# Kernel tuning notes

Hardware: AMD Instinct MI355X
Metric: run time of the kernel (lower is better)

## Reference

```python
import jax, jax.numpy as jnp
from jax import lax
import numpy as np

PAD = 1          # padding (pair, symmetric)
STRIDE = (1, 1)  # (strideY, strideX)
KH, KW = 3, 3
C_IN, C_OUT = 256, 512


def setup_inputs() -> dict:
    key = jax.random.key(0)
    k1, k2 = jax.random.split(key)
    x = jax.random.normal(k1, (1, C_IN, 256, 256), dtype=jnp.float32)
    # reset_parameters: uniform(-stdv, stdv), stdv = 1/sqrt(numel(weight))
    stdv = 1.0 / np.sqrt(C_OUT * C_IN * KH * KW)
    weight = jax.random.uniform(k2, (C_OUT, C_IN, KH, KW), dtype=jnp.float32,
                                minval=-stdv, maxval=stdv)
    return {"x": x, "weight": weight}


def reference(x, weight):
    # pad H and W with constant value 1 (as in module's pad())
    xp = jnp.pad(x, ((0, 0), (0, 0), (PAD, PAD), (PAD, PAD)), constant_values=1.0)
    # binarize input: (x >= 0) -> +1 else -1 (detached in torch; non-diff anyway)
    xb = jnp.where(xp >= 0, 1.0, -1.0).astype(x.dtype)
    # input_K: channel-mean of |x| then avg_pool2d(kernel, stride), VALID
    abs_mean = jnp.mean(jnp.abs(xp), axis=1)  # [B, Hp, Wp]
    k_sum = lax.reduce_window(abs_mean, 0.0, lax.add,
                              (1, KH, KW), (1,) + STRIDE, 'VALID')
    input_K = k_sum / (KH * KW)  # [B, Ho, Wo]
    # binary conv (real-valued emulation of XNOR+popcount)
    conv = lax.conv_general_dilated(xb, weight, window_strides=STRIDE,
                                    padding='VALID',
                                    dimension_numbers=('NCHW', 'OIHW', 'NCHW'))
    # weight_alpha: per-output-channel mean of weight (note: mean, not abs-mean,
    # in the training-path forward())
    alpha = jnp.mean(weight, axis=(1, 2, 3))  # [C_out]
    return conv * input_K[:, None, :, :] * alpha[None, :, None, None]
```

## Files before the change

### kernel.cpp

```cpp
#include <hip/hip_runtime.h>

typedef unsigned short UST;
typedef unsigned int u32;
typedef __attribute__((ext_vector_type(4))) int i32x4;

#define HPAD 258
#define CIN 256
#define COUT 512
#define KTOT 2304

#define SCALES_OFF (COUT * KTOT)
#define XBT_OFF    (SCALES_OFF + 2048)
#define XBT_BYTES  (HPAD * HPAD * CIN)
#define ABSM_OFF   (XBT_OFF + XBT_BYTES)
#define ABSM_BYTES (HPAD * HPAD * 4)
#define INK_OFF    (ABSM_OFF + ABSM_BYTES)

__device__ __forceinline__ void gload_lds16(const void* g, void* l) {
  __builtin_amdgcn_global_load_lds(
      (const __attribute__((address_space(1))) u32*)g,
      (__attribute__((address_space(3))) u32*)l, 16, 0, 0);
}

__global__ __launch_bounds__(256) void k_prep_w(const float* __restrict__ w,
                                                signed char* __restrict__ wq,
                                                float* __restrict__ scales) {
  int co = blockIdx.x;
  int ci = threadIdx.x;
  const float* wr = w + co * KTOT + ci * 9;
  float v[9];
  float s = 0.f, mx = 0.f;
#pragma unroll
  for (int j = 0; j < 9; ++j) {
    v[j] = wr[j]; s += v[j]; mx = fmaxf(mx, fabsf(v[j]));
  }
  __shared__ float redS[256];
  __shared__ float redM[256];
  redS[ci] = s; redM[ci] = mx;
  __syncthreads();
#pragma unroll
  for (int off = 128; off > 0; off >>= 1) {
    if (ci < off) {
      redS[ci] += redS[ci + off];
      redM[ci] = fmaxf(redM[ci], redM[ci + off]);
    }
    __syncthreads();
  }
  float alpha = redS[0] * (1.0f / 2304.0f);
  float maxw = redM[0];
  float inv = 127.0f / maxw;
  signed char* wo = wq + co * KTOT + ci;
#pragma unroll
  for (int j = 0; j < 9; ++j)
    wo[j * 256] = (signed char)__float2int_rn(v[j] * inv);
  if (ci == 0) scales[co] = alpha * maxw * (1.0f / 127.0f);
}

__global__ __launch_bounds__(256) void k_binz(const float* __restrict__ x,
                                              signed char* __restrict__ xbt,
                                              float* __restrict__ absm) {
  int hp = blockIdx.x;
  int wt = blockIdx.y;
  int wpl = threadIdx.x & 63;
  int chunk = threadIdx.x >> 6;
  int wp = wt * 64 + wpl;
  bool valid = wp < HPAD;
  int hx = hp - 1, wx = wp - 1;
  bool inb = valid && ((unsigned)hx < 256u) && ((unsigned)wx < 256u);
  float asum = 0.f;
  u32 pk[16];
#pragma unroll
  for (int c4 = 0; c4 < 16; ++c4) {
    u32 word = 0;
#pragma unroll
    for (int b = 0; b < 4; ++b) {
      int ci = chunk * 64 + c4 * 4 + b;
      float v = 1.0f;
      if (inb) v = x[(unsigned)ci * 65536u + (unsigned)(hx * 256 + wx)];
      asum += fabsf(v);
      u32 byte = (v >= 0.f) ? 0x01u : 0xFFu;
      word |= byte << (8 * b);
    }
    pk[c4] = word;
  }
  if (valid) {
    uint4* dst = (uint4*)(xbt + (unsigned)(hp * HPAD + wp) * 256u + chunk * 64);
#pragma unroll
    for (int g = 0; g < 4; ++g)
      dst[g] = make_uint4(pk[g * 4], pk[g * 4 + 1], pk[g * 4 + 2], pk[g * 4 + 3]);
  }
  __shared__ float red[4][64];
  red[chunk][wpl] = asum;
  __syncthreads();
  if (chunk == 0 && valid) {
    float tot = red[0][wpl] + red[1][wpl] + red[2][wpl] + red[3][wpl];
    absm[hp * HPAD + wp] = tot * (1.0f / 256.0f);
  }
}

__global__ __launch_bounds__(256) void k_inputk(const float* __restrict__ absm,
                                                float* __restrict__ inK) {
  int h = blockIdx.x, w = threadIdx.x;
  float s = 0.f;
#pragma unroll
  for (int dh = 0; dh < 3; ++dh)
#pragma unroll
    for (int dw = 0; dw < 3; ++dw) s += absm[(h + dh) * HPAD + (w + dw)];
  inK[h * 256 + w] = s * (1.0f / 9.0f);
}

#define MMI(a, b, c) __builtin_amdgcn_mfma_i32_16x16x64_i8(a, b, c, 0, 0, 0)

#define A_LDS(BUF) (lds + (BUF) * 32768)
#define B_LDS(BUF) (lds + 65536 + (BUF) * 32768)
#define RD_A(BUF, KS, M) (*(const i32x4*)(A_LDS(BUF) + swzA[KS][M]))
#define RD_B(BUF, KS, N) (*(const i32x4*)(B_LDS(BUF) + swzB[KS][N]))

#define STAGE_A(SRC, BUF) do { \
    char* d_ = A_LDS(BUF) + wv * 1024; \
    gload_lds16((SRC) + aoff[0], d_); \
    gload_lds16((SRC) + aoff[1], d_ + 8192); \
    gload_lds16((SRC) + aoff[2], d_ + 16384); \
    gload_lds16((SRC) + aoff[3], d_ + 24576); } while (0)

#define STAGE_B(SRC, BUF) do { \
    char* d_ = B_LDS(BUF) + wv * 1024; \
    gload_lds16((SRC) + boff[0], d_); \
    gload_lds16((SRC) + boff[1], d_ + 8192); \
    gload_lds16((SRC) + boff[2], d_ + 16384); \
    gload_lds16((SRC) + boff[3], d_ + 24576); } while (0)

#define SB __builtin_amdgcn_sched_barrier(0)

#define RD12(BUF, KS, BV, ALO, AHI) \
  BV[0] = RD_B(BUF, KS, 0); BV[1] = RD_B(BUF, KS, 1); \
  BV[2] = RD_B(BUF, KS, 2); BV[3] = RD_B(BUF, KS, 3); \
  ALO[0] = RD_A(BUF, KS, 0); ALO[1] = RD_A(BUF, KS, 1); \
  ALO[2] = RD_A(BUF, KS, 2); ALO[3] = RD_A(BUF, KS, 3); \
  AHI[0] = RD_A(BUF, KS, 4); AHI[1] = RD_A(BUF, KS, 5); \
  AHI[2] = RD_A(BUF, KS, 6); AHI[3] = RD_A(BUF, KS, 7);

#define MFMA32(ALO, AHI, BV) \
  __builtin_amdgcn_s_setprio(1); \
  _Pragma("unroll") for (int m = 0; m < 4; ++m) \
  _Pragma("unroll") for (int n = 0; n < 4; ++n) \
    acc[m][n] = MMI(ALO[m], BV[n], acc[m][n]); \
  _Pragma("unroll") for (int m = 0; m < 4; ++m) \
  _Pragma("unroll") for (int n = 0; n < 4; ++n) \
    acc[m + 4][n] = MMI(AHI[m], BV[n], acc[m + 4][n]); \
  __builtin_amdgcn_s_setprio(0);

#define BODY(CUR, ASRC, BSRC) do { \
  i32x4 b0[4], alo0[4], ahi0[4], b1[4], alo1[4], ahi1[4]; \
  RD12(CUR, 0, b0, alo0, ahi0); \
  STAGE_A((ASRC), (CUR) ^ 1); STAGE_B((BSRC), (CUR) ^ 1); \
  SB; MFMA32(alo0, ahi0, b0); SB; \
  RD12(CUR, 1, b1, alo1, ahi1); \
  SB; MFMA32(alo1, ahi1, b1); SB; \
  asm volatile("s_waitcnt vmcnt(0)" ::: "memory"); \
  __builtin_amdgcn_s_barrier(); \
} while (0)

#define BODY_LAST(CUR) do { \
  i32x4 b0[4], alo0[4], ahi0[4], b1[4], alo1[4], ahi1[4]; \
  RD12(CUR, 0, b0, alo0, ahi0); \
  SB; MFMA32(alo0, ahi0, b0); SB; \
  RD12(CUR, 1, b1, alo1, ahi1); \
  SB; MFMA32(alo1, ahi1, b1); SB; \
} while (0)

__global__ __launch_bounds__(512, 2) void k_conv8(const signed char* __restrict__ wq,
                                                  const signed char* __restrict__ xbt,
                                                  const float* __restrict__ scales,
                                                  const float* __restrict__ inK,
                                                  float* __restrict__ out) {
  __shared__ __align__(16) char lds[131072];
  int tid = threadIdx.x;
  int lane = tid & 63;
  int wv = tid >> 6;
  int wm = wv >> 2, wn = wv & 3;
  int bid = blockIdx.x;
  int bs = (bid & 7) * 64 + (bid >> 3);
  int mt = bs & 1;
  int h = bs >> 1;
  int co0 = mt << 8;

  int aoff[4], boff[4];
#pragma unroll
  for (int i = 0; i < 4; ++i) {
    u32 ql = (u32)(i * 512 + tid) * 16u;
    u32 row = ql >> 7;
    u32 s = (ql >> 4) & 7u;
    u32 slot = s ^ (row & 7u);
    aoff[i] = (int)((co0 + row) * 2304u + slot * 16u);
    boff[i] = (int)(row * 256u + slot * 16u);
  }
  int swzA[2][8], swzB[2][4];
#pragma unroll
  for (int ks = 0; ks < 2; ++ks) {
#pragma unroll
    for (int m = 0; m < 8; ++m) {
      u32 row = (u32)(wm * 128 + m * 16 + (lane & 15));
      u32 slot = (u32)(ks * 4 + (lane >> 4));
      swzA[ks][m] = (int)(row * 128u + (slot ^ (row & 7u)) * 16u);
    }
#pragma unroll
    for (int n = 0; n < 4; ++n) {
      u32 row = (u32)(wn * 64 + n * 16 + (lane & 15));
      u32 slot = (u32)(ks * 4 + (lane >> 4));
      swzB[ks][n] = (int)(row * 128u + (slot ^ (row & 7u)) * 16u);
    }
  }

  const char* wb_b = (const char*)wq;
  const char* xbt_b = (const char*)xbt;

  i32x4 acc[8][4];
#pragma unroll
  for (int m = 0; m < 8; ++m)
#pragma unroll
    for (int n = 0; n < 4; ++n) acc[m][n] = (i32x4){0, 0, 0, 0};

  STAGE_A(wb_b, 0);
  STAGE_B(xbt_b + (h * HPAD) * 256, 0);
  asm volatile("s_waitcnt vmcnt(0)" ::: "memory");
  __builtin_amdgcn_s_barrier();

#pragma unroll
  for (int t = 0; t < 17; ++t) {
    int tn = t + 1;
    int g = tn >> 1;
    int gh = g / 3, gw = g % 3;
    const char* asrc = wb_b + tn * 128;
    const char* bsrc = xbt_b + ((h + gh) * HPAD + gw) * 256 + (tn & 1) * 128;
    if (t & 1) { BODY(1, asrc, bsrc); }
    else       { BODY(0, asrc, bsrc); }
  }
  BODY_LAST(1);

  int col = lane & 15, rg = lane >> 4;
  int pixbase = h * 256;
#pragma unroll
  for (int n = 0; n < 4; ++n) {
    int w = wn * 64 + n * 16 + col;
    float kv = inK[pixbase + w];
#pragma unroll
    for (int m = 0; m < 8; ++m) {
      int cobase = co0 + wm * 128 + m * 16 + rg * 4;
      float4 scv = *(const float4*)(scales + cobase);
      float* o = out + (u32)cobase * 65536u + (u32)(pixbase + w);
      o[0]          = (float)acc[m][n][0] * scv.x * kv;
      o[65536u]     = (float)acc[m][n][1] * scv.y * kv;
      o[2u * 65536u] = (float)acc[m][n][2] * scv.z * kv;
      o[3u * 65536u] = (float)acc[m][n][3] * scv.w * kv;
    }
  }
}

extern "C" void kernel_launch(void* const* d_in, const int* in_sizes, int n_in,
                              void* d_out, int out_size, void* d_ws, size_t ws_size,
                              hipStream_t stream) {
  const float* x = (const float*)d_in[0];
  const float* w = (const float*)d_in[1];
  float* out = (float*)d_out;
  char* ws = (char*)d_ws;
  signed char* wq = (signed char*)ws;
  float* scales = (float*)(ws + SCALES_OFF);
  signed char* xbt = (signed char*)(ws + XBT_OFF);
  float* absm = (float*)(ws + ABSM_OFF);
  float* inK = (float*)(ws + INK_OFF);

  k_prep_w<<<COUT, 256, 0, stream>>>(w, wq, scales);
  k_binz<<<dim3(HPAD, 5), 256, 0, stream>>>(x, xbt, absm);
  k_inputk<<<256, 256, 0, stream>>>(absm, inK);
  k_conv8<<<512, 512, 0, stream>>>(wq, xbt, scales, inK, out);
}
```

Before: 110.3 us.

## Deepen conv LDS pipeline with triple-buffered B and interleaved fragment reads

Restructures the int8 MFMA main loop in the conv kernel. The B (activation) tile is now triple-buffered in a larger 160KB LDS, and next-step fragment reads are interleaved between MFMA halves. The barrier waits only for older loads (vmcnt(4)) instead of draining all global loads. Because of the larger LDS footprint, launch bounds drop to one 512-thread block per CU, which trades occupancy for deeper prefetch and less stall per step.

After: 108.6 us. Within noise of the previous version (-1.6%).

```diff
diff --git a/kernel.cpp b/kernel.cpp
--- a/kernel.cpp
+++ b/kernel.cpp
@@ -111,70 +111,106 @@
 
 #define MMI(a, b, c) __builtin_amdgcn_mfma_i32_16x16x64_i8(a, b, c, 0, 0, 0)
 
-#define A_LDS(BUF) (lds + (BUF) * 32768)
-#define B_LDS(BUF) (lds + 65536 + (BUF) * 32768)
-#define RD_A(BUF, KS, M) (*(const i32x4*)(A_LDS(BUF) + swzA[KS][M]))
-#define RD_B(BUF, KS, N) (*(const i32x4*)(B_LDS(BUF) + swzB[KS][N]))
-
-#define STAGE_A(SRC, BUF) do { \
-    char* d_ = A_LDS(BUF) + wv * 1024; \
+#define A_LDS(S) (lds + (S) * 32768)
+#define B_LDS(S) (lds + 65536 + (S) * 32768)
+#define RD_A(S, KS, M) (*(const i32x4*)(A_LDS(S) + swzA[KS][M]))
+#define RD_B(S, KS, N) (*(const i32x4*)(B_LDS(S) + swzB[KS][N]))
+
+#define STAGE_A(SRC, S) do { \
+    char* d_ = A_LDS(S) + wv * 1024; \
     gload_lds16((SRC) + aoff[0], d_); \
     gload_lds16((SRC) + aoff[1], d_ + 8192); \
     gload_lds16((SRC) + aoff[2], d_ + 16384); \
     gload_lds16((SRC) + aoff[3], d_ + 24576); } while (0)
 
-#define STAGE_B(SRC, BUF) do { \
-    char* d_ = B_LDS(BUF) + wv * 1024; \
+#define STAGE_B(SRC, S) do { \
+    char* d_ = B_LDS(S) + wv * 1024; \
     gload_lds16((SRC) + boff[0], d_); \
     gload_lds16((SRC) + boff[1], d_ + 8192); \
     gload_lds16((SRC) + boff[2], d_ + 16384); \
     gload_lds16((SRC) + boff[3], d_ + 24576); } while (0)
 
 #define SB __builtin_amdgcn_sched_barrier(0)
-
-#define RD12(BUF, KS, BV, ALO, AHI) \
-  BV[0] = RD_B(BUF, KS, 0); BV[1] = RD_B(BUF, KS, 1); \
-  BV[2] = RD_B(BUF, KS, 2); BV[3] = RD_B(BUF, KS, 3); \
-  ALO[0] = RD_A(BUF, KS, 0); ALO[1] = RD_A(BUF, KS, 1); \
-  ALO[2] = RD_A(BUF, KS, 2); ALO[3] = RD_A(BUF, KS, 3); \
-  AHI[0] = RD_A(BUF, KS, 4); AHI[1] = RD_A(BUF, KS, 5); \
-  AHI[2] = RD_A(BUF, KS, 6); AHI[3] = RD_A(BUF, KS, 7);
-
-#define MFMA32(ALO, AHI, BV) \
+#define VMW(N) asm volatile("s_waitcnt vmcnt(" #N ")" ::: "memory")
+#define LGK0 asm volatile("s_waitcnt lgkmcnt(0)" ::: "memory")
+
+#define RDB4(S, KS, D) \
+  D[0] = RD_B(S, KS, 0); D[1] = RD_B(S, KS, 1); \
+  D[2] = RD_B(S, KS, 2); D[3] = RD_B(S, KS, 3);
+#define RDALO(S, KS, D) \
+  D[0] = RD_A(S, KS, 0); D[1] = RD_A(S, KS, 1); \
+  D[2] = RD_A(S, KS, 2); D[3] = RD_A(S, KS, 3);
+#define RDAHI(S, KS, D) \
+  D[0] = RD_A(S, KS, 4); D[1] = RD_A(S, KS, 5); \
+  D[2] = RD_A(S, KS, 6); D[3] = RD_A(S, KS, 7);
+
+#define MF_LO(AA, BB) \
   __builtin_amdgcn_s_setprio(1); \
   _Pragma("unroll") for (int m = 0; m < 4; ++m) \
   _Pragma("unroll") for (int n = 0; n < 4; ++n) \
-    acc[m][n] = MMI(ALO[m], BV[n], acc[m][n]); \
+    acc[m][n] = MMI(AA[m], BB[n], acc[m][n]); \
+  __builtin_amdgcn_s_setprio(0);
+#define MF_HI(AA, BB) \
+  __builtin_amdgcn_s_setprio(1); \
   _Pragma("unroll") for (int m = 0; m < 4; ++m) \
   _Pragma("unroll") for (int n = 0; n < 4; ++n) \
-    acc[m + 4][n] = MMI(AHI[m], BV[n], acc[m + 4][n]); \
+    acc[m + 4][n] = MMI(AA[m], BB[n], acc[m + 4][n]); \
   __builtin_amdgcn_s_setprio(0);
 
-#define BODY(CUR, ASRC, BSRC) do { \
-  i32x4 b0[4], alo0[4], ahi0[4], b1[4], alo1[4], ahi1[4]; \
-  RD12(CUR, 0, b0, alo0, ahi0); \
-  STAGE_A((ASRC), (CUR) ^ 1); STAGE_B((BSRC), (CUR) ^ 1); \
-  SB; MFMA32(alo0, ahi0, b0); SB; \
-  RD12(CUR, 1, b1, alo1, ahi1); \
-  SB; MFMA32(alo1, ahi1, b1); SB; \
-  asm volatile("s_waitcnt vmcnt(0)" ::: "memory"); \
+#define BGPX(TT) (xbt_b + ((h + ((TT) >> 1) / 3) * HPAD + (((TT) >> 1) % 3)) * 256 \
+                  + ((TT) & 1) * 128)
+
+#define BODY(CA, CB, SA, SBT, TA, TB, ASRC, BSRC) do { \
+  i32x4 Ahi_[4], B1_[4], A1lo_[4], A1hi_[4]; \
+  RDAHI(CA, 0, Ahi_); \
+  STAGE_A((ASRC), SA); STAGE_B((BSRC), SBT); \
+  SB; MF_LO(Alo_, B0_); SB; \
+  RDB4(CB, 1, B1_); RDALO(CA, 1, A1lo_); \
+  SB; MF_HI(Ahi_, B0_); SB; \
+  RDAHI(CA, 1, A1hi_); \
+  SB; MF_LO(A1lo_, B1_); SB; \
+  LGK0; VMW(4); \
   __builtin_amdgcn_s_barrier(); \
+  RDB4(TB, 0, B0_); RDALO(TA, 0, Alo_); \
+  SB; MF_HI(A1hi_, B1_); SB; \
 } while (0)
 
-#define BODY_LAST(CUR) do { \
-  i32x4 b0[4], alo0[4], ahi0[4], b1[4], alo1[4], ahi1[4]; \
-  RD12(CUR, 0, b0, alo0, ahi0); \
-  SB; MFMA32(alo0, ahi0, b0); SB; \
-  RD12(CUR, 1, b1, alo1, ahi1); \
-  SB; MFMA32(alo1, ahi1, b1); SB; \
+#define BU(U) BODY((U) & 1, (U) % 3, ((U) + 1) & 1, ((U) + 2) % 3, \
+                   ((U) + 1) & 1, ((U) + 1) % 3, \
+                   wb_b + ((U) + 1) * 128, BGPX((U) + 2))
+
+#define BODY16() do { \
+  i32x4 Ahi_[4], B1_[4], A1lo_[4], A1hi_[4]; \
+  RDAHI(0, 0, Ahi_); \
+  STAGE_A(wb_b + 17 * 128, 1); \
+  SB; MF_LO(Alo_, B0_); SB; \
+  RDB4(1, 1, B1_); RDALO(0, 1, A1lo_); \
+  SB; MF_HI(Ahi_, B0_); SB; \
+  RDAHI(0, 1, A1hi_); \
+  SB; MF_LO(A1lo_, B1_); SB; \
+  LGK0; VMW(0); \
+  __builtin_amdgcn_s_barrier(); \
+  RDB4(2, 0, B0_); RDALO(1, 0, Alo_); \
+  SB; MF_HI(A1hi_, B1_); SB; \
 } while (0)
 
-__global__ __launch_bounds__(512, 2) void k_conv8(const signed char* __restrict__ wq,
+#define BODY17() do { \
+  i32x4 Ahi_[4], B1_[4], A1lo_[4], A1hi_[4]; \
+  RDAHI(1, 0, Ahi_); \
+  SB; MF_LO(Alo_, B0_); SB; \
+  RDB4(2, 1, B1_); RDALO(1, 1, A1lo_); \
+  SB; MF_HI(Ahi_, B0_); SB; \
+  RDAHI(1, 1, A1hi_); \
+  SB; MF_LO(A1lo_, B1_); SB; \
+  SB; MF_HI(A1hi_, B1_); SB; \
+} while (0)
+
+__global__ __launch_bounds__(512, 1) void k_conv8(const signed char* __restrict__ wq,
                                                   const signed char* __restrict__ xbt,
                                                   const float* __restrict__ scales,
                                                   const float* __restrict__ inK,
                                                   float* __restrict__ out) {
-  __shared__ __align__(16) char lds[131072];
+  __shared__ __align__(16) char lds[163840];
   int tid = threadIdx.x;
   int lane = tid & 63;
   int wv = tid >> 6;
@@ -221,22 +257,19 @@
 #pragma unroll
     for (int n = 0; n < 4; ++n) acc[m][n] = (i32x4){0, 0, 0, 0};
 
+  i32x4 B0_[4], Alo_[4];
+
   STAGE_A(wb_b, 0);
-  STAGE_B(xbt_b + (h * HPAD) * 256, 0);
-  asm volatile("s_waitcnt vmcnt(0)" ::: "memory");
+  STAGE_B(BGPX(0), 0);
+  STAGE_B(BGPX(1), 1);
+  VMW(4);
   __builtin_amdgcn_s_barrier();
-
-#pragma unroll
-  for (int t = 0; t < 17; ++t) {
-    int tn = t + 1;
-    int g = tn >> 1;
-    int gh = g / 3, gw = g % 3;
-    const char* asrc = wb_b + tn * 128;
-    const char* bsrc = xbt_b + ((h + gh) * HPAD + gw) * 256 + (tn & 1) * 128;
-    if (t & 1) { BODY(1, asrc, bsrc); }
-    else       { BODY(0, asrc, bsrc); }
-  }
-  BODY_LAST(1);
+  RDB4(0, 0, B0_); RDALO(0, 0, Alo_);
+
+  BU(0); BU(1); BU(2); BU(3); BU(4); BU(5); BU(6); BU(7);
+  BU(8); BU(9); BU(10); BU(11); BU(12); BU(13); BU(14); BU(15);
+  BODY16();
+  BODY17();
 
   int col = lane & 15, rg = lane >> 4;
   int pixbase = h * 256;
@@ -249,8 +282,8 @@
       int cobase = co0 + wm * 128 + m * 16 + rg * 4;
       float4 scv = *(const float4*)(scales + cobase);
       float* o = out + (u32)cobase * 65536u + (u32)(pixbase + w);
-      o[0]          = (float)acc[m][n][0] * scv.x * kv;
-      o[65536u]     = (float)acc[m][n][1] * scv.y * kv;
+      o[0]           = (float)acc[m][n][0] * scv.x * kv;
+      o[65536u]      = (float)acc[m][n][1] * scv.y * kv;
       o[2u * 65536u] = (float)acc[m][n][2] * scv.z * kv;
       o[3u * 65536u] = (float)acc[m][n][3] * scv.w * kv;
     }
```
